# Kernel optimization log

Hardware: AMD Instinct MI355X
Metric: run time of the kernel (lower is better)

Reference implementation:

```python
import jax, jax.numpy as jnp
import numpy as np

B, L, N, D, C, WS, NH = 32, 64, 1024, 512, 8192, 3, 16
HD = D // NH          # head_dim = 32
HID = 2 * D           # MLP expansion = 2


def _ln(x, g, b, eps=1e-5):
    m = jnp.mean(x, -1, keepdims=True)
    v = jnp.mean((x - m) ** 2, -1, keepdims=True)
    return (x - m) * jax.lax.rsqrt(v + eps) * g + b


def setup_inputs() -> dict:
    key = jax.random.key(0)
    ks = jax.random.split(key, 16)
    r = lambda i, shape, s=0.02: jax.random.normal(ks[i], shape, jnp.float32) * s
    return dict(
        visual_features=jax.random.normal(ks[0], (B, N, D), jnp.float32),
        targets=jax.random.randint(ks[1], (B, L), 0, C),
        pad_id=1,
        char_embed=r(2, (C, D), 1.0),
        ln1_g=jnp.ones(D), ln1_b=jnp.zeros(D),
        in_proj_w=r(3, (3 * D, D)), in_proj_b=jnp.zeros(3 * D),
        out_w=r(4, (D, D)), out_b=jnp.zeros(D),
        fc1_w=r(5, (HID, D)), fc1_b=jnp.zeros(HID),
        fc2_w=r(6, (D, HID)), fc2_b=jnp.zeros(D),
        ln2_g=jnp.ones(D), ln2_b=jnp.zeros(D),
        left_token=r(7, (1, 1, D)), right_token=r(8, (1, 1, D)),
        q_w=r(9, (D, D)), q_b=jnp.zeros(D),
        kv_w=r(10, (2 * D, D)), kv_b=jnp.zeros(2 * D),
        proj_w=r(11, (D, D)), proj_b=jnp.zeros(D),
        lnq_g=jnp.ones(D), lnq_b=jnp.zeros(D),
        lnkv_g=jnp.ones(D), lnkv_b=jnp.zeros(D),
        head_w=r(12, (C, D)), head_b=jnp.zeros(C),
    )


def reference(visual_features, targets, pad_id, char_embed, ln1_g, ln1_b,
              in_proj_w, in_proj_b, out_w, out_b, fc1_w, fc1_b, fc2_w, fc2_b,
              ln2_g, ln2_b, left_token, right_token, q_w, q_b, kv_w, kv_b,
              proj_w, proj_b, lnq_g, lnq_b, lnkv_g, lnkv_b, head_w, head_b):
    # --- build left/right context windows via gather (vectorizes the python loop) ---
    padded = jnp.pad(targets, ((0, 0), (WS, WS)), constant_values=pad_id)
    li = jnp.arange(L)[:, None] + jnp.arange(WS)[None, :]      # (L, WS)
    left_ids = padded[:, li]                                   # (B, L, WS)
    right_ids = padded[:, li + WS + 1]                         # (B, L, WS)

    def encode(ids, tok):
        x = char_embed[ids] + tok                 # (B, L, WS, D)
        x = x.reshape(B * L, WS, D)               # (M, WS, D)
        xn = _ln(x, ln1_g, ln1_b)
        qkv = xn @ in_proj_w.T + in_proj_b
        q, k, v = jnp.split(qkv, 3, -1)
        sh = lambda t: t.reshape(B * L, WS, NH, HD).transpose(0, 2, 1, 3)
        q, k, v = sh(q), sh(k), sh(v)
        a = jax.nn.softmax(jnp.einsum('mhqd,mhkd->mhqk', q, k) * HD ** -0.5, -1)
        o = jnp.einsum('mhqk,mhkd->mhqd', a, v).transpose(0, 2, 1, 3).reshape(B * L, WS, D)
        x = x + o @ out_w.T + out_b
        h = jax.nn.gelu(_ln(x, ln2_g, ln2_b) @ fc1_w.T + fc1_b, approximate=False)
        x = x + h @ fc2_w.T + fc2_b
        return x.mean(1).reshape(B, L, D)

    def cross(qs):
        q = _ln(qs, lnq_g, lnq_b) @ q_w.T + q_b
        kv = _ln(visual_features, lnkv_g, lnkv_b) @ kv_w.T + kv_b
        k, v = jnp.split(kv, 2, -1)
        q = q.reshape(B, L, NH, HD).transpose(0, 2, 1, 3)
        k = k.reshape(B, N, NH, HD).transpose(0, 2, 1, 3)
        v = v.reshape(B, N, NH, HD).transpose(0, 2, 1, 3)
        a = jax.nn.softmax(jnp.einsum('bhld,bhnd->bhln', q, k) * HD ** -0.5, -1)
        o = jnp.einsum('bhln,bhnd->bhld', a, v).transpose(0, 2, 1, 3).reshape(B, L, D)
        return o @ proj_w.T + proj_b

    left_enc = encode(left_ids, left_token)
    right_enc = encode(right_ids, right_token)
    left_feat = left_enc + cross(left_enc)
    right_feat = right_enc + cross(right_enc)
    sgm_left = left_feat @ head_w.T + head_b      # (B, L, C)
    sgm_right = right_feat @ head_w.T + head_b    # (B, L, C)
    return sgm_left, sgm_right, targets
```

## Files before the change

### kernel.cpp

```cpp
#include <hip/hip_runtime.h>
#include <hip/hip_bf16.h>
#include <cstdint>
#include <cstddef>


typedef __attribute__((ext_vector_type(8))) short s16x8;
typedef __attribute__((ext_vector_type(8))) unsigned short u16x8;
typedef __attribute__((ext_vector_type(4))) unsigned short u16x4;
typedef __attribute__((ext_vector_type(4))) float f32x4;

__device__ __forceinline__ float b2f(unsigned short u) {
  union { unsigned int i; float f; } c; c.i = ((unsigned int)u) << 16; return c.f;
}
__device__ __forceinline__ unsigned short f2b(float f) {
  union { float f; unsigned int i; } c; c.f = f;
  unsigned int x = c.i;
  return (unsigned short)((x + 0x7FFFu + ((x >> 16) & 1u)) >> 16);
}

#define GLOAD16(gp, lp)                                                        \
  __builtin_amdgcn_global_load_lds(                                           \
      (const __attribute__((address_space(1))) void*)(gp),                    \
      (__attribute__((address_space(3))) void*)(lp), 16, 0, 0)

__global__ void cvt_f32_bf16(const float* __restrict__ s, unsigned short* __restrict__ d, int n4) {
  int i = blockIdx.x * 256 + threadIdx.x;
  if (i >= n4) return;
  float4 v = ((const float4*)s)[i];
  u16x4 o; o[0] = f2b(v.x); o[1] = f2b(v.y); o[2] = f2b(v.z); o[3] = f2b(v.w);
  *(u16x4*)(d + (size_t)i * 4) = o;
}

__global__ void embed_k(const int* __restrict__ targets, const int* __restrict__ pad_p,
                        const float* __restrict__ ce, const float* __restrict__ ltok,
                        const float* __restrict__ rtok, float* __restrict__ x) {
  int idx = blockIdx.x * 256 + threadIdx.x;
  if (idx >= 12288 * 128) return;
  int row = idx >> 7, d4 = idx & 127;
  int side = row >= 6144;
  int rem = row - side * 6144;
  int pos = rem / 3, w = rem - pos * 3;
  int b = pos >> 6, l = pos & 63;
  int id;
  if (!side) { int ti = l + w - 3; id = (ti >= 0) ? targets[(b << 6) + ti] : *pad_p; }
  else       { int ti = l + w + 1; id = (ti < 64) ? targets[(b << 6) + ti] : *pad_p; }
  float4 cv = ((const float4*)ce)[(size_t)id * 128 + d4];
  float4 tv = ((const float4*)(side ? rtok : ltok))[d4];
  float4 o; o.x = cv.x + tv.x; o.y = cv.y + tv.y; o.z = cv.z + tv.z; o.w = cv.w + tv.w;
  ((float4*)x)[idx] = o;
}

__global__ __launch_bounds__(256) void ln_rows(const float* __restrict__ in,
    const float* __restrict__ g, const float* __restrict__ b,
    unsigned short* __restrict__ out, int M) {
  int row = blockIdx.x * 4 + (threadIdx.x >> 6);
  int lane = threadIdx.x & 63;
  const float* rp = in + (size_t)row * 512;
  float4 v0 = ((const float4*)rp)[lane * 2];
  float4 v1 = ((const float4*)rp)[lane * 2 + 1];
  float vv[8] = {v0.x, v0.y, v0.z, v0.w, v1.x, v1.y, v1.z, v1.w};
  float s = 0.f, ss = 0.f;
#pragma unroll
  for (int j = 0; j < 8; ++j) { s += vv[j]; ss += vv[j] * vv[j]; }
#pragma unroll
  for (int o = 1; o < 64; o <<= 1) { s += __shfl_xor(s, o); ss += __shfl_xor(ss, o); }
  float mean = s * (1.0f / 512.0f);
  float var = ss * (1.0f / 512.0f) - mean * mean;
  float inv = rsqrtf(var + 1e-5f);
  int c = lane * 8;
  u16x8 o8;
#pragma unroll
  for (int j = 0; j < 8; ++j) o8[j] = f2b((vv[j] - mean) * inv * g[c + j] + b[c + j]);
  *(u16x8*)(out + (size_t)row * 512 + c) = o8;
}

template<int RES, int GELU, int OUTBF, int KVT>
__global__ __launch_bounds__(256) void gemm_bt(
    const unsigned short* __restrict__ A, const unsigned short* __restrict__ Bt,
    const float* __restrict__ bias, const float* __restrict__ res,
    void* __restrict__ outp, int M, int N, int K) {
  __shared__ unsigned short sA[128 * 32];
  __shared__ unsigned short sB[128 * 32];
  const int tid = threadIdx.x;
  const int nbx = gridDim.x;
  int id = blockIdx.y * nbx + blockIdx.x;
  {
    const int nwg = nbx * gridDim.y;
    if ((nwg & 7) == 0) id = (id & 7) * (nwg >> 3) + (id >> 3);
  }
  const int bm = (id / nbx) * 128, bn = (id % nbx) * 128;
  const int wave = tid >> 6, lane = tid & 63;
  const int wr = (wave >> 1) * 64, wc = (wave & 1) * 64;
  const int lrow = lane & 15, lk = (lane >> 4) * 8;
  f32x4 acc[4][4] = {};
  const int srow = lane >> 2;
  const int scol = (lane & 3) * 8;
  const unsigned short* gA0 = A + (size_t)(bm + wave * 32 + srow) * K + scol;
  const unsigned short* gA1 = gA0 + (size_t)16 * K;
  const unsigned short* gB0 = Bt + (size_t)(bn + wave * 32 + srow) * K + scol;
  const unsigned short* gB1 = gB0 + (size_t)16 * K;
  unsigned short* lA0 = &sA[wave * 1024];
  unsigned short* lA1 = &sA[wave * 1024 + 512];
  unsigned short* lB0 = &sB[wave * 1024];
  unsigned short* lB1 = &sB[wave * 1024 + 512];
  for (int k0 = 0; k0 < K; k0 += 32) {
    __syncthreads();
    GLOAD16(gA0 + k0, lA0);
    GLOAD16(gA1 + k0, lA1);
    GLOAD16(gB0 + k0, lB0);
    GLOAD16(gB1 + k0, lB1);
    __syncthreads();
    s16x8 av[4], bv[4];
#pragma unroll
    for (int m = 0; m < 4; ++m) av[m] = *(const s16x8*)&sA[(wr + m * 16 + lrow) * 32 + lk];
#pragma unroll
    for (int n = 0; n < 4; ++n) bv[n] = *(const s16x8*)&sB[(wc + n * 16 + lrow) * 32 + lk];
#pragma unroll
    for (int m = 0; m < 4; ++m)
#pragma unroll
      for (int n = 0; n < 4; ++n)
        acc[m][n] = __builtin_amdgcn_mfma_f32_16x16x32_bf16(av[m], bv[n], acc[m][n], 0, 0, 0);
  }
  const int orow0 = bm + wr + (lane >> 4) * 4;
  const int ocol0 = bn + wc + (lane & 15);
#pragma unroll
  for (int m = 0; m < 4; ++m) {
#pragma unroll
    for (int n = 0; n < 4; ++n) {
#pragma unroll
      for (int r = 0; r < 4; ++r) {
        int row = orow0 + m * 16 + r;
        int col = ocol0 + n * 16;
        float v = acc[m][n][r] + bias[col];
        if (KVT) {
          int bb = row >> 10, nn = row & 1023;
          unsigned short* Kp = (unsigned short*)outp;
          unsigned short* VpT = Kp + 16777216u;
          if (col < 512) {
            int hh = col >> 5, dd = col & 31;
            Kp[(((size_t)(bb * 16 + hh)) * 1024 + nn) * 32 + dd] = f2b(v);
          } else {
            int cc = col - 512, hh = cc >> 5, dd = cc & 31;
            VpT[(((size_t)(bb * 16 + hh)) * 32 + dd) * 1024 + nn] = f2b(v);
          }
        } else {
          if (GELU) v = 0.5f * v * (1.0f + erff(v * 0.70710678118654752f));
          if (RES) v += res[(size_t)row * N + col];
          if (OUTBF) ((unsigned short*)outp)[(size_t)row * N + col] = f2b(v);
          else       ((float*)outp)[(size_t)row * N + col] = v;
        }
      }
    }
  }
}

__global__ __launch_bounds__(256) void winattn(const unsigned short* __restrict__ qkv,
                                               unsigned short* __restrict__ o) {
  int g = blockIdx.x * 256 + threadIdx.x;
  if (g >= 4096 * 48) return;
  int i = g % 3;
  int t = g / 3;
  int h = t & 15;
  int sp = t >> 4;
  const unsigned short* base = qkv + (size_t)sp * 4608 + h * 32;
  float qv[32];
  {
    const u16x8* qp = (const u16x8*)(base + (size_t)i * 1536);
#pragma unroll
    for (int c = 0; c < 4; ++c) {
      u16x8 v = qp[c];
#pragma unroll
      for (int j = 0; j < 8; ++j) qv[c * 8 + j] = b2f(v[j]);
    }
  }
  float s[3];
#pragma unroll
  for (int j3 = 0; j3 < 3; ++j3) {
    const u16x8* kp = (const u16x8*)(base + (size_t)j3 * 1536 + 512);
    float acc = 0.f;
#pragma unroll
    for (int c = 0; c < 4; ++c) {
      u16x8 v = kp[c];
#pragma unroll
      for (int j = 0; j < 8; ++j) acc += qv[c * 8 + j] * b2f(v[j]);
    }
    s[j3] = acc * 0.17677669529663687f;
  }
  float mx = fmaxf(s[0], fmaxf(s[1], s[2]));
  float e0 = __expf(s[0] - mx), e1 = __expf(s[1] - mx), e2 = __expf(s[2] - mx);
  float inv = 1.0f / (e0 + e1 + e2);
  float a0 = e0 * inv, a1 = e1 * inv, a2 = e2 * inv;
  unsigned short* op = o + (size_t)(sp * 3 + i) * 512 + h * 32;
  const u16x8* v0p = (const u16x8*)(base + 1024);
  const u16x8* v1p = (const u16x8*)(base + 1536 + 1024);
  const u16x8* v2p = (const u16x8*)(base + 3072 + 1024);
#pragma unroll
  for (int c = 0; c < 4; ++c) {
    u16x8 x0 = v0p[c], x1 = v1p[c], x2 = v2p[c];
    u16x8 ov;
#pragma unroll
    for (int j = 0; j < 8; ++j)
      ov[j] = f2b(a0 * b2f(x0[j]) + a1 * b2f(x1[j]) + a2 * b2f(x2[j]));
    *(u16x8*)(op + c * 8) = ov;
  }
}

__global__ void mean3(const float* __restrict__ x, float* __restrict__ enc) {
  int i = blockIdx.x * 256 + threadIdx.x;
  if (i >= 4096 * 128) return;
  int p = i >> 7, d4 = i & 127;
  const float4* xp = (const float4*)x;
  float4 a = xp[(size_t)(p * 3 + 0) * 128 + d4];
  float4 b = xp[(size_t)(p * 3 + 1) * 128 + d4];
  float4 c = xp[(size_t)(p * 3 + 2) * 128 + d4];
  float4 o;
  o.x = (a.x + b.x + c.x) * (1.0f / 3.0f);
  o.y = (a.y + b.y + c.y) * (1.0f / 3.0f);
  o.z = (a.z + b.z + c.z) * (1.0f / 3.0f);
  o.w = (a.w + b.w + c.w) * (1.0f / 3.0f);
  ((float4*)enc)[i] = o;
}

__global__ __launch_bounds__(256) void crossattn_mfma(const float* __restrict__ q,
    const unsigned short* __restrict__ Kp, const unsigned short* __restrict__ VpT,
    unsigned short* __restrict__ o) {
  __shared__ unsigned short Plds[4][2][16 * 40];
  const int sbh = blockIdx.x;
  const int side = sbh >> 9, b = (sbh >> 4) & 31, h = sbh & 15;
  const int tid = threadIdx.x;
  const int w = tid >> 6, lane = tid & 63;
  const int ql = lane & 15, g = lane >> 4;
  const int qrow = side * 2048 + b * 64 + w * 16 + ql;
  const float SC = 0.17677669529663687f;
  s16x8 qf;
  {
    const float* qp = q + (size_t)qrow * 512 + h * 32 + g * 8;
    float4 qa = ((const float4*)qp)[0];
    float4 qb4 = ((const float4*)qp)[1];
    qf[0] = (short)f2b(qa.x * SC); qf[1] = (short)f2b(qa.y * SC);
    qf[2] = (short)f2b(qa.z * SC); qf[3] = (short)f2b(qa.w * SC);
    qf[4] = (short)f2b(qb4.x * SC); qf[5] = (short)f2b(qb4.y * SC);
    qf[6] = (short)f2b(qb4.z * SC); qf[7] = (short)f2b(qb4.w * SC);
  }
  const unsigned short* kbase = Kp + ((size_t)(b * 16 + h) * 1024) * 32;
  const unsigned short* vbase = VpT + ((size_t)(b * 16 + h) * 32) * 1024;
  f32x4 oacc0 = {}, oacc1 = {};
  float m_run = -1e30f, l_part = 0.f;
  for (int kv0 = 0; kv0 < 1024; kv0 += 32) {
    const int pp = (kv0 >> 5) & 1;
    s16x8 kf0 = *(const s16x8*)(kbase + (size_t)(kv0 + ql) * 32 + g * 8);
    s16x8 kf1 = *(const s16x8*)(kbase + (size_t)(kv0 + 16 + ql) * 32 + g * 8);
    f32x4 z = {0.f, 0.f, 0.f, 0.f};
    f32x4 s0 = __builtin_amdgcn_mfma_f32_16x16x32_bf16(kf0, qf, z, 0, 0, 0);
    f32x4 s1 = __builtin_amdgcn_mfma_f32_16x16x32_bf16(kf1, qf, z, 0, 0, 0);
    float cm = fmaxf(fmaxf(fmaxf(s0[0], s0[1]), fmaxf(s0[2], s0[3])),
                     fmaxf(fmaxf(s1[0], s1[1]), fmaxf(s1[2], s1[3])));
    cm = fmaxf(cm, __shfl_xor(cm, 16));
    cm = fmaxf(cm, __shfl_xor(cm, 32));
    float m_new = fmaxf(m_run, cm);
    float corr = __expf(m_run - m_new);
    m_run = m_new;
    float p0[4], p1[4], ps = 0.f;
#pragma unroll
    for (int r = 0; r < 4; ++r) {
      p0[r] = __expf(s0[r] - m_new);
      p1[r] = __expf(s1[r] - m_new);
      ps += p0[r] + p1[r];
    }
    l_part = l_part * corr + ps;
    oacc0 *= corr; oacc1 *= corr;
    u16x4 w0, w1;
#pragma unroll
    for (int r = 0; r < 4; ++r) { w0[r] = f2b(p0[r]); w1[r] = f2b(p1[r]); }
    *(u16x4*)&Plds[w][pp][ql * 40 + g * 4] = w0;
    *(u16x4*)&Plds[w][pp][ql * 40 + 16 + g * 4] = w1;
    __syncthreads();
    s16x8 pf = *(const s16x8*)&Plds[w][pp][ql * 40 + g * 8];
    s16x8 vf0 = *(const s16x8*)(vbase + (size_t)ql * 1024 + kv0 + g * 8);
    s16x8 vf1 = *(const s16x8*)(vbase + (size_t)(16 + ql) * 1024 + kv0 + g * 8);
    oacc0 = __builtin_amdgcn_mfma_f32_16x16x32_bf16(vf0, pf, oacc0, 0, 0, 0);
    oacc1 = __builtin_amdgcn_mfma_f32_16x16x32_bf16(vf1, pf, oacc1, 0, 0, 0);
  }
  float lf = l_part;
  lf += __shfl_xor(lf, 16);
  lf += __shfl_xor(lf, 32);
  float inv = 1.0f / lf;
  unsigned short* op = o + (size_t)qrow * 512 + h * 32;
  u16x4 ov0, ov1;
#pragma unroll
  for (int r = 0; r < 4; ++r) {
    ov0[r] = f2b(oacc0[r] * inv);
    ov1[r] = f2b(oacc1[r] * inv);
  }
  *(u16x4*)(op + g * 4) = ov0;
  *(u16x4*)(op + 16 + g * 4) = ov1;
}

__global__ void tail_targets(const int* __restrict__ t, float* __restrict__ out) {
  int i = blockIdx.x * 256 + threadIdx.x;
  if (i < 2048) out[33554432 + i] = (float)t[i];
}

extern "C" void kernel_launch(void* const* d_in, const int* in_sizes, int n_in,
                              void* d_out, int out_size, void* d_ws, size_t ws_size,
                              hipStream_t stream) {
  const float* visual   = (const float*)d_in[0];
  const int*   targets  = (const int*)d_in[1];
  const int*   pad_p    = (const int*)d_in[2];
  const float* char_emb = (const float*)d_in[3];
  const float* ln1_g = (const float*)d_in[4];
  const float* ln1_b = (const float*)d_in[5];
  const float* in_proj_w = (const float*)d_in[6];
  const float* in_proj_b = (const float*)d_in[7];
  const float* out_w = (const float*)d_in[8];
  const float* out_b = (const float*)d_in[9];
  const float* fc1_w = (const float*)d_in[10];
  const float* fc1_b = (const float*)d_in[11];
  const float* fc2_w = (const float*)d_in[12];
  const float* fc2_b = (const float*)d_in[13];
  const float* ln2_g = (const float*)d_in[14];
  const float* ln2_b = (const float*)d_in[15];
  const float* ltok  = (const float*)d_in[16];
  const float* rtok  = (const float*)d_in[17];
  const float* q_w   = (const float*)d_in[18];
  const float* q_b   = (const float*)d_in[19];
  const float* kv_w  = (const float*)d_in[20];
  const float* kv_b  = (const float*)d_in[21];
  const float* proj_w = (const float*)d_in[22];
  const float* proj_b = (const float*)d_in[23];
  const float* lnq_g = (const float*)d_in[24];
  const float* lnq_b = (const float*)d_in[25];
  const float* lnkv_g = (const float*)d_in[26];
  const float* lnkv_b = (const float*)d_in[27];
  const float* head_w = (const float*)d_in[28];
  const float* head_b = (const float*)d_in[29];

  char* ws = (char*)d_ws;
  unsigned short* W    = (unsigned short*)ws;
  float*          X    = (float*)(ws + 14680064ull);
  unsigned short* KP   = (unsigned short*)(ws + 14680064ull);
  unsigned short* A1   = (unsigned short*)(ws + 39845888ull);
  unsigned short* B1   = (unsigned short*)(ws + 52428800ull);
  unsigned short* QKV  = (unsigned short*)(ws + 77594624ull);
  float*          ENC  = (float*)(ws + 115343360ull);
  unsigned short* VIS  = (unsigned short*)(ws + 123731968ull);
  float*          Q    = (float*)(ws + 157286400ull);
  unsigned short* OC   = (unsigned short*)(ws + 165675008ull);
  unsigned short* FEAT = (unsigned short*)(ws + 169869312ull);
  unsigned short* LNQ  = (unsigned short*)(ws + 174063616ull);
  unsigned short* VPT  = KP + 16777216u;

  unsigned short* Wip   = W;
  unsigned short* Wout  = W + 786432;
  unsigned short* Wfc1  = W + 1048576;
  unsigned short* Wfc2  = W + 1572864;
  unsigned short* Wq    = W + 2097152;
  unsigned short* Wkv   = W + 2359296;
  unsigned short* Wproj = W + 2883584;
  unsigned short* Whead = W + 3145728;

  auto cvt = [&](const float* s, unsigned short* d, int n) {
    cvt_f32_bf16<<<dim3((n / 4 + 255) / 256), dim3(256), 0, stream>>>(s, d, n / 4);
  };
  cvt(in_proj_w, Wip, 786432);
  cvt(out_w, Wout, 262144);
  cvt(fc1_w, Wfc1, 524288);
  cvt(fc2_w, Wfc2, 524288);
  cvt(q_w, Wq, 262144);
  cvt(kv_w, Wkv, 524288);
  cvt(proj_w, Wproj, 262144);
  cvt(head_w, Whead, 4194304);

  embed_k<<<dim3(6144), dim3(256), 0, stream>>>(targets, pad_p, char_emb, ltok, rtok, X);
  ln_rows<<<dim3(3072), dim3(256), 0, stream>>>(X, ln1_g, ln1_b, A1, 12288);
  gemm_bt<0,0,1,0><<<dim3(12, 96), dim3(256), 0, stream>>>(A1, Wip, in_proj_b, nullptr, QKV, 12288, 1536, 512);
  winattn<<<dim3(768), dim3(256), 0, stream>>>(QKV, B1);
  gemm_bt<1,0,0,0><<<dim3(4, 96), dim3(256), 0, stream>>>(B1, Wout, out_b, X, X, 12288, 512, 512);
  ln_rows<<<dim3(3072), dim3(256), 0, stream>>>(X, ln2_g, ln2_b, A1, 12288);
  gemm_bt<0,1,1,0><<<dim3(8, 96), dim3(256), 0, stream>>>(A1, Wfc1, fc1_b, nullptr, B1, 12288, 1024, 512);
  gemm_bt<1,0,0,0><<<dim3(4, 96), dim3(256), 0, stream>>>(B1, Wfc2, fc2_b, X, X, 12288, 512, 1024);
  mean3<<<dim3(2048), dim3(256), 0, stream>>>(X, ENC);

  ln_rows<<<dim3(8192), dim3(256), 0, stream>>>(visual, lnkv_g, lnkv_b, VIS, 32768);
  gemm_bt<0,0,1,1><<<dim3(8, 256), dim3(256), 0, stream>>>(VIS, Wkv, kv_b, nullptr, KP, 32768, 1024, 512);
  ln_rows<<<dim3(1024), dim3(256), 0, stream>>>(ENC, lnq_g, lnq_b, LNQ, 4096);
  gemm_bt<0,0,0,0><<<dim3(4, 32), dim3(256), 0, stream>>>(LNQ, Wq, q_b, nullptr, Q, 4096, 512, 512);
  crossattn_mfma<<<dim3(1024), dim3(256), 0, stream>>>(Q, KP, VPT, OC);
  gemm_bt<1,0,1,0><<<dim3(4, 32), dim3(256), 0, stream>>>(OC, Wproj, proj_b, ENC, FEAT, 4096, 512, 512);

  gemm_bt<0,0,0,0><<<dim3(64, 32), dim3(256), 0, stream>>>(FEAT, Whead, head_b, nullptr, (float*)d_out, 4096, 8192, 512);
  tail_targets<<<dim3(8), dim3(256), 0, stream>>>(targets, (float*)d_out);
}
```

Measured before the change: 446.3 us.

## Pipeline GEMM LDS loads with 4-stage ring buffer and XOR swizzle

The bf16 GEMM mainloop moves from a single LDS buffer with two barriers per K-step to a 4-slot ring buffer that prefetches three tiles ahead. Explicit vmcnt waits and one barrier per step replace the earlier synchronisation. The LDS layout is XOR-swizzled to cut bank conflicts on the MFMA fragment reads, and s_setprio raises wave priority around the MFMA block. LDS use grows fourfold to 64KB per block, which may lower occupancy.

```diff
diff --git a/kernel.cpp b/kernel.cpp
--- a/kernel.cpp
+++ b/kernel.cpp
@@ -79,8 +79,8 @@
     const unsigned short* __restrict__ A, const unsigned short* __restrict__ Bt,
     const float* __restrict__ bias, const float* __restrict__ res,
     void* __restrict__ outp, int M, int N, int K) {
-  __shared__ unsigned short sA[128 * 32];
-  __shared__ unsigned short sB[128 * 32];
+  __shared__ unsigned short sA[4][128 * 32];
+  __shared__ unsigned short sB[4][128 * 32];
   const int tid = threadIdx.x;
   const int nbx = gridDim.x;
   int id = blockIdx.y * nbx + blockIdx.x;
@@ -91,35 +91,50 @@
   const int bm = (id / nbx) * 128, bn = (id % nbx) * 128;
   const int wave = tid >> 6, lane = tid & 63;
   const int wr = (wave >> 1) * 64, wc = (wave & 1) * 64;
-  const int lrow = lane & 15, lk = (lane >> 4) * 8;
+  const int lrow = lane & 15;
+  const int c8 = (((lane >> 4) ^ ((lane >> 1) & 3)) << 3);
   f32x4 acc[4][4] = {};
   const int srow = lane >> 2;
-  const int scol = (lane & 3) * 8;
-  const unsigned short* gA0 = A + (size_t)(bm + wave * 32 + srow) * K + scol;
+  const int swcol = (((lane & 3) ^ ((lane >> 3) & 3)) << 3);
+  const unsigned short* gA0 = A + (size_t)(bm + wave * 32 + srow) * K + swcol;
   const unsigned short* gA1 = gA0 + (size_t)16 * K;
-  const unsigned short* gB0 = Bt + (size_t)(bn + wave * 32 + srow) * K + scol;
+  const unsigned short* gB0 = Bt + (size_t)(bn + wave * 32 + srow) * K + swcol;
   const unsigned short* gB1 = gB0 + (size_t)16 * K;
-  unsigned short* lA0 = &sA[wave * 1024];
-  unsigned short* lA1 = &sA[wave * 1024 + 512];
-  unsigned short* lB0 = &sB[wave * 1024];
-  unsigned short* lB1 = &sB[wave * 1024 + 512];
-  for (int k0 = 0; k0 < K; k0 += 32) {
-    __syncthreads();
-    GLOAD16(gA0 + k0, lA0);
-    GLOAD16(gA1 + k0, lA1);
-    GLOAD16(gB0 + k0, lB0);
-    GLOAD16(gB1 + k0, lB1);
-    __syncthreads();
+  const int lbase = wave * 1024;
+  const int NT = K >> 5;
+#pragma unroll
+  for (int t = 0; t < 3; ++t) {
+    GLOAD16(gA0 + t * 32, &sA[t][lbase]);
+    GLOAD16(gA1 + t * 32, &sA[t][lbase + 512]);
+    GLOAD16(gB0 + t * 32, &sB[t][lbase]);
+    GLOAD16(gB1 + t * 32, &sB[t][lbase + 512]);
+  }
+  for (int t = 0; t < NT; ++t) {
+    if (t <= NT - 3)      asm volatile("s_waitcnt vmcnt(8)" ::: "memory");
+    else if (t == NT - 2) asm volatile("s_waitcnt vmcnt(4)" ::: "memory");
+    else                  asm volatile("s_waitcnt vmcnt(0)" ::: "memory");
+    __builtin_amdgcn_s_barrier();
+    __builtin_amdgcn_sched_barrier(0);
+    if (t + 3 < NT) {
+      const int s = t + 3, sl = s & 3;
+      GLOAD16(gA0 + s * 32, &sA[sl][lbase]);
+      GLOAD16(gA1 + s * 32, &sA[sl][lbase + 512]);
+      GLOAD16(gB0 + s * 32, &sB[sl][lbase]);
+      GLOAD16(gB1 + s * 32, &sB[sl][lbase + 512]);
+    }
+    const int cur = t & 3;
     s16x8 av[4], bv[4];
 #pragma unroll
-    for (int m = 0; m < 4; ++m) av[m] = *(const s16x8*)&sA[(wr + m * 16 + lrow) * 32 + lk];
-#pragma unroll
-    for (int n = 0; n < 4; ++n) bv[n] = *(const s16x8*)&sB[(wc + n * 16 + lrow) * 32 + lk];
+    for (int m = 0; m < 4; ++m) av[m] = *(const s16x8*)&sA[cur][(wr + m * 16 + lrow) * 32 + c8];
+#pragma unroll
+    for (int n = 0; n < 4; ++n) bv[n] = *(const s16x8*)&sB[cur][(wc + n * 16 + lrow) * 32 + c8];
+    __builtin_amdgcn_s_setprio(1);
 #pragma unroll
     for (int m = 0; m < 4; ++m)
 #pragma unroll
       for (int n = 0; n < 4; ++n)
         acc[m][n] = __builtin_amdgcn_mfma_f32_16x16x32_bf16(av[m], bv[n], acc[m][n], 0, 0, 0);
+    __builtin_amdgcn_s_setprio(0);
   }
   const int orow0 = bm + wr + (lane >> 4) * 4;
   const int ocol0 = bn + wc + (lane & 15);
```

Measured after the change: 451.3 us. No clear change (+1.1%).

## Replace 128x128 GEMM with double-buffered 256x256 tile, BK=64, XOR-swizzled LDS

Applied to the files above, without the earlier changes.

The bf16 GEMM moves from 128x128 tiles with 256 threads and BK=32 to 256x256 tiles with 512 threads and BK=64. It double-buffers LDS so global-to-LDS loads of the next K tile overlap MFMA work, and XOR-swizzles the LDS layout to avoid bank conflicts. The goals are more reuse per byte loaded, fewer barriers per MFMA and hidden load latency. In exchange it uses 128 KB of LDS per block, allowing only one block per CU. Small GEMMs (M=4096, N=512) now launch only 32 blocks, which may leave most of the CUs idle.

```diff
diff --git a/kernel.cpp b/kernel.cpp
--- a/kernel.cpp
+++ b/kernel.cpp
@@ -75,12 +75,12 @@
 }
 
 template<int RES, int GELU, int OUTBF, int KVT>
-__global__ __launch_bounds__(256) void gemm_bt(
+__global__ __launch_bounds__(512) void gemm256(
     const unsigned short* __restrict__ A, const unsigned short* __restrict__ Bt,
     const float* __restrict__ bias, const float* __restrict__ res,
     void* __restrict__ outp, int M, int N, int K) {
-  __shared__ unsigned short sA[128 * 32];
-  __shared__ unsigned short sB[128 * 32];
+  __shared__ unsigned short sA[2][256 * 64];
+  __shared__ unsigned short sB[2][256 * 64];
   const int tid = threadIdx.x;
   const int nbx = gridDim.x;
   int id = blockIdx.y * nbx + blockIdx.x;
@@ -88,43 +88,55 @@
     const int nwg = nbx * gridDim.y;
     if ((nwg & 7) == 0) id = (id & 7) * (nwg >> 3) + (id >> 3);
   }
-  const int bm = (id / nbx) * 128, bn = (id % nbx) * 128;
+  const int bm = (id / nbx) * 256, bn = (id % nbx) * 256;
   const int wave = tid >> 6, lane = tid & 63;
-  const int wr = (wave >> 1) * 64, wc = (wave & 1) * 64;
-  const int lrow = lane & 15, lk = (lane >> 4) * 8;
-  f32x4 acc[4][4] = {};
-  const int srow = lane >> 2;
-  const int scol = (lane & 3) * 8;
-  const unsigned short* gA0 = A + (size_t)(bm + wave * 32 + srow) * K + scol;
-  const unsigned short* gA1 = gA0 + (size_t)16 * K;
-  const unsigned short* gB0 = Bt + (size_t)(bn + wave * 32 + srow) * K + scol;
-  const unsigned short* gB1 = gB0 + (size_t)16 * K;
-  unsigned short* lA0 = &sA[wave * 1024];
-  unsigned short* lA1 = &sA[wave * 1024 + 512];
-  unsigned short* lB0 = &sB[wave * 1024];
-  unsigned short* lB1 = &sB[wave * 1024 + 512];
-  for (int k0 = 0; k0 < K; k0 += 32) {
+  const int wr = (wave >> 2) * 128, wc = (wave & 3) * 64;
+  const int lrow = lane & 15, g = lane >> 4;
+  const int xr = lrow & 7;
+  f32x4 acc[8][4] = {};
+  const int sr = tid >> 3;
+  const int sc = (((tid & 7) ^ (sr & 7)) << 3);
+  const unsigned short* gA = A + (size_t)(bm + sr) * K + sc;
+  const unsigned short* gB = Bt + (size_t)(bn + sr) * K + sc;
+  const int NT = K >> 6;
+
+#define STAGE256(buf, kt)                                                      \
+  {                                                                            \
+    _Pragma("unroll")                                                          \
+    for (int i = 0; i < 4; ++i) {                                              \
+      GLOAD16(gA + (size_t)(i * 64) * K + (kt) * 64, &sA[buf][i * 4096 + wave * 512]); \
+      GLOAD16(gB + (size_t)(i * 64) * K + (kt) * 64, &sB[buf][i * 4096 + wave * 512]); \
+    }                                                                          \
+  }
+
+  STAGE256(0, 0);
+  __syncthreads();
+  int cur = 0;
+  for (int kt = 0; kt < NT; ++kt) {
+    if (kt + 1 < NT) STAGE256(cur ^ 1, kt + 1);
+#pragma unroll
+    for (int kh = 0; kh < 2; ++kh) {
+      const int pc = ((kh * 4 + g) ^ xr) << 3;
+      s16x8 av[8], bv[4];
+#pragma unroll
+      for (int m = 0; m < 8; ++m) av[m] = *(const s16x8*)&sA[cur][(wr + m * 16 + lrow) * 64 + pc];
+#pragma unroll
+      for (int n = 0; n < 4; ++n) bv[n] = *(const s16x8*)&sB[cur][(wc + n * 16 + lrow) * 64 + pc];
+#pragma unroll
+      for (int m = 0; m < 8; ++m)
+#pragma unroll
+        for (int n = 0; n < 4; ++n)
+          acc[m][n] = __builtin_amdgcn_mfma_f32_16x16x32_bf16(av[m], bv[n], acc[m][n], 0, 0, 0);
+    }
     __syncthreads();
-    GLOAD16(gA0 + k0, lA0);
-    GLOAD16(gA1 + k0, lA1);
-    GLOAD16(gB0 + k0, lB0);
-    GLOAD16(gB1 + k0, lB1);
-    __syncthreads();
-    s16x8 av[4], bv[4];
-#pragma unroll
-    for (int m = 0; m < 4; ++m) av[m] = *(const s16x8*)&sA[(wr + m * 16 + lrow) * 32 + lk];
-#pragma unroll
-    for (int n = 0; n < 4; ++n) bv[n] = *(const s16x8*)&sB[(wc + n * 16 + lrow) * 32 + lk];
-#pragma unroll
-    for (int m = 0; m < 4; ++m)
-#pragma unroll
-      for (int n = 0; n < 4; ++n)
-        acc[m][n] = __builtin_amdgcn_mfma_f32_16x16x32_bf16(av[m], bv[n], acc[m][n], 0, 0, 0);
-  }
-  const int orow0 = bm + wr + (lane >> 4) * 4;
-  const int ocol0 = bn + wc + (lane & 15);
-#pragma unroll
-  for (int m = 0; m < 4; ++m) {
+    cur ^= 1;
+  }
+#undef STAGE256
+
+  const int orow0 = bm + wr + g * 4;
+  const int ocol0 = bn + wc + lrow;
+#pragma unroll
+  for (int m = 0; m < 8; ++m) {
 #pragma unroll
     for (int n = 0; n < 4; ++n) {
 #pragma unroll
@@ -373,21 +385,21 @@
 
   embed_k<<<dim3(6144), dim3(256), 0, stream>>>(targets, pad_p, char_emb, ltok, rtok, X);
   ln_rows<<<dim3(3072), dim3(256), 0, stream>>>(X, ln1_g, ln1_b, A1, 12288);
-  gemm_bt<0,0,1,0><<<dim3(12, 96), dim3(256), 0, stream>>>(A1, Wip, in_proj_b, nullptr, QKV, 12288, 1536, 512);
+  gemm256<0,0,1,0><<<dim3(6, 48), dim3(512), 0, stream>>>(A1, Wip, in_proj_b, nullptr, QKV, 12288, 1536, 512);
   winattn<<<dim3(768), dim3(256), 0, stream>>>(QKV, B1);
-  gemm_bt<1,0,0,0><<<dim3(4, 96), dim3(256), 0, stream>>>(B1, Wout, out_b, X, X, 12288, 512, 512);
+  gemm256<1,0,0,0><<<dim3(2, 48), dim3(512), 0, stream>>>(B1, Wout, out_b, X, X, 12288, 512, 512);
   ln_rows<<<dim3(3072), dim3(256), 0, stream>>>(X, ln2_g, ln2_b, A1, 12288);
-  gemm_bt<0,1,1,0><<<dim3(8, 96), dim3(256), 0, stream>>>(A1, Wfc1, fc1_b, nullptr, B1, 12288, 1024, 512);
-  gemm_bt<1,0,0,0><<<dim3(4, 96), dim3(256), 0, stream>>>(B1, Wfc2, fc2_b, X, X, 12288, 512, 1024);
+  gemm256<0,1,1,0><<<dim3(4, 48), dim3(512), 0, stream>>>(A1, Wfc1, fc1_b, nullptr, B1, 12288, 1024, 512);
+  gemm256<1,0,0,0><<<dim3(2, 48), dim3(512), 0, stream>>>(B1, Wfc2, fc2_b, X, X, 12288, 512, 1024);
   mean3<<<dim3(2048), dim3(256), 0, stream>>>(X, ENC);
 
   ln_rows<<<dim3(8192), dim3(256), 0, stream>>>(visual, lnkv_g, lnkv_b, VIS, 32768);
-  gemm_bt<0,0,1,1><<<dim3(8, 256), dim3(256), 0, stream>>>(VIS, Wkv, kv_b, nullptr, KP, 32768, 1024, 512);
+  gemm256<0,0,1,1><<<dim3(4, 128), dim3(512), 0, stream>>>(VIS, Wkv, kv_b, nullptr, KP, 32768, 1024, 512);
   ln_rows<<<dim3(1024), dim3(256), 0, stream>>>(ENC, lnq_g, lnq_b, LNQ, 4096);
-  gemm_bt<0,0,0,0><<<dim3(4, 32), dim3(256), 0, stream>>>(LNQ, Wq, q_b, nullptr, Q, 4096, 512, 512);
+  gemm256<0,0,0,0><<<dim3(2, 16), dim3(512), 0, stream>>>(LNQ, Wq, q_b, nullptr, Q, 4096, 512, 512);
   crossattn_mfma<<<dim3(1024), dim3(256), 0, stream>>>(Q, KP, VPT, OC);
-  gemm_bt<1,0,1,0><<<dim3(4, 32), dim3(256), 0, stream>>>(OC, Wproj, proj_b, ENC, FEAT, 4096, 512, 512);
-
-  gemm_bt<0,0,0,0><<<dim3(64, 32), dim3(256), 0, stream>>>(FEAT, Whead, head_b, nullptr, (float*)d_out, 4096, 8192, 512);
+  gemm256<1,0,1,0><<<dim3(2, 16), dim3(512), 0, stream>>>(OC, Wproj, proj_b, ENC, FEAT, 4096, 512, 512);
+
+  gemm256<0,0,0,0><<<dim3(32, 16), dim3(512), 0, stream>>>(FEAT, Whead, head_b, nullptr, (float*)d_out, 4096, 8192, 512);
   tail_targets<<<dim3(8), dim3(256), 0, stream>>>(targets, (float*)d_out);
 }
```

Result: slower. 582.5 us (+30.5%).

## Double-buffer GEMM LDS tiles with swizzled layout, BK=64, and vectorized epilogue

Applied to the files above, without the earlier changes.

Rewrites the shared bf16 GEMM kernel used by every projection. It double-buffers LDS with a K-tile of 64 so the global-to-LDS loads for the next tile overlap the MFMAs on the current one, and it drops one barrier per iteration. It also XOR-swizzles the LDS layout to cut bank conflicts and raises wave priority around the MFMA blocks. The operands are swapped so each lane holds four consecutive output columns, which allows vector bias, residual and output accesses in the epilogue. The cost is four times the LDS per block, which may lower occupancy.

```diff
diff --git a/kernel.cpp b/kernel.cpp
--- a/kernel.cpp
+++ b/kernel.cpp
@@ -75,12 +75,12 @@
 }
 
 template<int RES, int GELU, int OUTBF, int KVT>
-__global__ __launch_bounds__(256) void gemm_bt(
+__global__ __launch_bounds__(256) void gemm128(
     const unsigned short* __restrict__ A, const unsigned short* __restrict__ Bt,
     const float* __restrict__ bias, const float* __restrict__ res,
     void* __restrict__ outp, int M, int N, int K) {
-  __shared__ unsigned short sA[128 * 32];
-  __shared__ unsigned short sB[128 * 32];
+  __shared__ unsigned short sA[2][8192];
+  __shared__ unsigned short sB[2][8192];
   const int tid = threadIdx.x;
   const int nbx = gridDim.x;
   int id = blockIdx.y * nbx + blockIdx.x;
@@ -91,64 +91,104 @@
   const int bm = (id / nbx) * 128, bn = (id % nbx) * 128;
   const int wave = tid >> 6, lane = tid & 63;
   const int wr = (wave >> 1) * 64, wc = (wave & 1) * 64;
-  const int lrow = lane & 15, lk = (lane >> 4) * 8;
+  const int lrow = lane & 15, g = lane >> 4;
   f32x4 acc[4][4] = {};
-  const int srow = lane >> 2;
-  const int scol = (lane & 3) * 8;
-  const unsigned short* gA0 = A + (size_t)(bm + wave * 32 + srow) * K + scol;
-  const unsigned short* gA1 = gA0 + (size_t)16 * K;
-  const unsigned short* gB0 = Bt + (size_t)(bn + wave * 32 + srow) * K + scol;
-  const unsigned short* gB1 = gB0 + (size_t)16 * K;
-  unsigned short* lA0 = &sA[wave * 1024];
-  unsigned short* lA1 = &sA[wave * 1024 + 512];
-  unsigned short* lB0 = &sB[wave * 1024];
-  unsigned short* lB1 = &sB[wave * 1024 + 512];
-  for (int k0 = 0; k0 < K; k0 += 32) {
+  const int xoff = (((((lrow & 1) << 2) | g) ^ ((lrow >> 1) & 7)) << 3);
+  const int baseA = ((wr >> 1) + (lrow >> 1)) * 64 + xoff;
+  const int baseB = ((wc >> 1) + (lrow >> 1)) * 64 + xoff;
+  const int slot8 = (tid & 7) ^ ((tid >> 3) & 7);
+  const int srow = ((tid >> 3) << 1) + (slot8 >> 2);
+  const int scol = (slot8 & 3) << 3;
+  const unsigned short* gA = A + (size_t)(bm + srow) * K + scol;
+  const unsigned short* gB = Bt + (size_t)(bn + srow) * K + scol;
+  const int NT = K >> 6;
+
+#define STAGE128(buf, kt)                                                      \
+  { _Pragma("unroll")                                                          \
+    for (int h = 0; h < 2; ++h) {                                              \
+      _Pragma("unroll")                                                        \
+      for (int i = 0; i < 2; ++i) {                                            \
+        GLOAD16(gA + (size_t)(i * 64) * K + (kt) * 64 + h * 32,                \
+                &sA[buf][h * 4096 + i * 2048 + wave * 512]);                   \
+        GLOAD16(gB + (size_t)(i * 64) * K + (kt) * 64 + h * 32,                \
+                &sB[buf][h * 4096 + i * 2048 + wave * 512]);                   \
+      }                                                                        \
+    } }
+
+  STAGE128(0, 0);
+  __syncthreads();
+  int cur = 0;
+  for (int kt = 0; kt < NT; ++kt) {
+    s16x8 a0[4], b0[4];
+#pragma unroll
+    for (int m = 0; m < 4; ++m) a0[m] = *(const s16x8*)&sA[cur][baseA + m * 512];
+#pragma unroll
+    for (int n = 0; n < 4; ++n) b0[n] = *(const s16x8*)&sB[cur][baseB + n * 512];
+    if (kt + 1 < NT) STAGE128(cur ^ 1, kt + 1);
+    __builtin_amdgcn_s_setprio(1);
+#pragma unroll
+    for (int m = 0; m < 4; ++m)
+#pragma unroll
+      for (int n = 0; n < 4; ++n)
+        acc[m][n] = __builtin_amdgcn_mfma_f32_16x16x32_bf16(b0[n], a0[m], acc[m][n], 0, 0, 0);
+    __builtin_amdgcn_s_setprio(0);
+    s16x8 a1[4], b1[4];
+#pragma unroll
+    for (int m = 0; m < 4; ++m) a1[m] = *(const s16x8*)&sA[cur][4096 + baseA + m * 512];
+#pragma unroll
+    for (int n = 0; n < 4; ++n) b1[n] = *(const s16x8*)&sB[cur][4096 + baseB + n * 512];
+    __builtin_amdgcn_s_setprio(1);
+#pragma unroll
+    for (int m = 0; m < 4; ++m)
+#pragma unroll
+      for (int n = 0; n < 4; ++n)
+        acc[m][n] = __builtin_amdgcn_mfma_f32_16x16x32_bf16(b1[n], a1[m], acc[m][n], 0, 0, 0);
+    __builtin_amdgcn_s_setprio(0);
     __syncthreads();
-    GLOAD16(gA0 + k0, lA0);
-    GLOAD16(gA1 + k0, lA1);
-    GLOAD16(gB0 + k0, lB0);
-    GLOAD16(gB1 + k0, lB1);
-    __syncthreads();
-    s16x8 av[4], bv[4];
-#pragma unroll
-    for (int m = 0; m < 4; ++m) av[m] = *(const s16x8*)&sA[(wr + m * 16 + lrow) * 32 + lk];
-#pragma unroll
-    for (int n = 0; n < 4; ++n) bv[n] = *(const s16x8*)&sB[(wc + n * 16 + lrow) * 32 + lk];
-#pragma unroll
-    for (int m = 0; m < 4; ++m)
-#pragma unroll
-      for (int n = 0; n < 4; ++n)
-        acc[m][n] = __builtin_amdgcn_mfma_f32_16x16x32_bf16(av[m], bv[n], acc[m][n], 0, 0, 0);
-  }
-  const int orow0 = bm + wr + (lane >> 4) * 4;
-  const int ocol0 = bn + wc + (lane & 15);
+    cur ^= 1;
+  }
+#undef STAGE128
+
+  const int orow_ = bm + wr + lrow;
+  const int ocol_ = bn + wc + g * 4;
 #pragma unroll
   for (int m = 0; m < 4; ++m) {
+    const int row = orow_ + m * 16;
 #pragma unroll
     for (int n = 0; n < 4; ++n) {
-#pragma unroll
-      for (int r = 0; r < 4; ++r) {
-        int row = orow0 + m * 16 + r;
-        int col = ocol0 + n * 16;
-        float v = acc[m][n][r] + bias[col];
-        if (KVT) {
-          int bb = row >> 10, nn = row & 1023;
-          unsigned short* Kp = (unsigned short*)outp;
-          unsigned short* VpT = Kp + 16777216u;
-          if (col < 512) {
-            int hh = col >> 5, dd = col & 31;
-            Kp[(((size_t)(bb * 16 + hh)) * 1024 + nn) * 32 + dd] = f2b(v);
-          } else {
-            int cc = col - 512, hh = cc >> 5, dd = cc & 31;
-            VpT[(((size_t)(bb * 16 + hh)) * 32 + dd) * 1024 + nn] = f2b(v);
-          }
+      const int col = ocol_ + n * 16;
+      f32x4 v = acc[m][n];
+      f32x4 b4 = *(const f32x4*)(bias + col);
+      v += b4;
+      if (GELU) {
+#pragma unroll
+        for (int r = 0; r < 4; ++r)
+          v[r] = 0.5f * v[r] * (1.0f + erff(v[r] * 0.70710678118654752f));
+      }
+      if (RES) v += *(const f32x4*)(res + (size_t)row * N + col);
+      if (KVT) {
+        int bb = row >> 10, nn = row & 1023;
+        unsigned short* Kp = (unsigned short*)outp;
+        unsigned short* VpT = Kp + 16777216u;
+        if (col < 512) {
+          int hh = col >> 5, dd = col & 31;
+          u16x4 o4;
+#pragma unroll
+          for (int r = 0; r < 4; ++r) o4[r] = f2b(v[r]);
+          *(u16x4*)(Kp + (((size_t)(bb * 16 + hh)) * 1024 + nn) * 32 + dd) = o4;
         } else {
-          if (GELU) v = 0.5f * v * (1.0f + erff(v * 0.70710678118654752f));
-          if (RES) v += res[(size_t)row * N + col];
-          if (OUTBF) ((unsigned short*)outp)[(size_t)row * N + col] = f2b(v);
-          else       ((float*)outp)[(size_t)row * N + col] = v;
+          int cc = col - 512, hh = cc >> 5, dd = cc & 31;
+#pragma unroll
+          for (int r = 0; r < 4; ++r)
+            VpT[(((size_t)(bb * 16 + hh)) * 32 + dd + r) * 1024 + nn] = f2b(v[r]);
         }
+      } else if (OUTBF) {
+        u16x4 o4;
+#pragma unroll
+        for (int r = 0; r < 4; ++r) o4[r] = f2b(v[r]);
+        *(u16x4*)((unsigned short*)outp + (size_t)row * N + col) = o4;
+      } else {
+        *(f32x4*)((float*)outp + (size_t)row * N + col) = v;
       }
     }
   }
@@ -373,21 +413,21 @@
 
   embed_k<<<dim3(6144), dim3(256), 0, stream>>>(targets, pad_p, char_emb, ltok, rtok, X);
   ln_rows<<<dim3(3072), dim3(256), 0, stream>>>(X, ln1_g, ln1_b, A1, 12288);
-  gemm_bt<0,0,1,0><<<dim3(12, 96), dim3(256), 0, stream>>>(A1, Wip, in_proj_b, nullptr, QKV, 12288, 1536, 512);
+  gemm128<0,0,1,0><<<dim3(12, 96), dim3(256), 0, stream>>>(A1, Wip, in_proj_b, nullptr, QKV, 12288, 1536, 512);
   winattn<<<dim3(768), dim3(256), 0, stream>>>(QKV, B1);
-  gemm_bt<1,0,0,0><<<dim3(4, 96), dim3(256), 0, stream>>>(B1, Wout, out_b, X, X, 12288, 512, 512);
+  gemm128<1,0,0,0><<<dim3(4, 96), dim3(256), 0, stream>>>(B1, Wout, out_b, X, X, 12288, 512, 512);
   ln_rows<<<dim3(3072), dim3(256), 0, stream>>>(X, ln2_g, ln2_b, A1, 12288);
-  gemm_bt<0,1,1,0><<<dim3(8, 96), dim3(256), 0, stream>>>(A1, Wfc1, fc1_b, nullptr, B1, 12288, 1024, 512);
-  gemm_bt<1,0,0,0><<<dim3(4, 96), dim3(256), 0, stream>>>(B1, Wfc2, fc2_b, X, X, 12288, 512, 1024);
+  gemm128<0,1,1,0><<<dim3(8, 96), dim3(256), 0, stream>>>(A1, Wfc1, fc1_b, nullptr, B1, 12288, 1024, 512);
+  gemm128<1,0,0,0><<<dim3(4, 96), dim3(256), 0, stream>>>(B1, Wfc2, fc2_b, X, X, 12288, 512, 1024);
   mean3<<<dim3(2048), dim3(256), 0, stream>>>(X, ENC);
 
   ln_rows<<<dim3(8192), dim3(256), 0, stream>>>(visual, lnkv_g, lnkv_b, VIS, 32768);
-  gemm_bt<0,0,1,1><<<dim3(8, 256), dim3(256), 0, stream>>>(VIS, Wkv, kv_b, nullptr, KP, 32768, 1024, 512);
+  gemm128<0,0,1,1><<<dim3(8, 256), dim3(256), 0, stream>>>(VIS, Wkv, kv_b, nullptr, KP, 32768, 1024, 512);
   ln_rows<<<dim3(1024), dim3(256), 0, stream>>>(ENC, lnq_g, lnq_b, LNQ, 4096);
-  gemm_bt<0,0,0,0><<<dim3(4, 32), dim3(256), 0, stream>>>(LNQ, Wq, q_b, nullptr, Q, 4096, 512, 512);
+  gemm128<0,0,0,0><<<dim3(4, 32), dim3(256), 0, stream>>>(LNQ, Wq, q_b, nullptr, Q, 4096, 512, 512);
   crossattn_mfma<<<dim3(1024), dim3(256), 0, stream>>>(Q, KP, VPT, OC);
-  gemm_bt<1,0,1,0><<<dim3(4, 32), dim3(256), 0, stream>>>(OC, Wproj, proj_b, ENC, FEAT, 4096, 512, 512);
-
-  gemm_bt<0,0,0,0><<<dim3(64, 32), dim3(256), 0, stream>>>(FEAT, Whead, head_b, nullptr, (float*)d_out, 4096, 8192, 512);
+  gemm128<1,0,1,0><<<dim3(4, 32), dim3(256), 0, stream>>>(OC, Wproj, proj_b, ENC, FEAT, 4096, 512, 512);
+
+  gemm128<0,0,0,0><<<dim3(64, 32), dim3(256), 0, stream>>>(FEAT, Whead, head_b, nullptr, (float*)d_out, 4096, 8192, 512);
   tail_targets<<<dim3(8), dim3(256), 0, stream>>>(targets, (float*)d_out);
 }
```

New measurement: 404.0 us. -9.5%, faster.
